# Kernel tuning notes

Hardware: AMD Instinct MI355X
Metric: run time of the kernel (lower is better)

Reference implementation:

```python
import jax, jax.numpy as jnp
import numpy as np

MAX_DISP = 4  # max_displacement
PAD = MAX_DISP
ODIM = 2 * MAX_DISP + 1  # 9 -> 81 cost-volume channels


def setup_inputs() -> dict:
    key = jax.random.key(0)
    k1, k2 = jax.random.split(key)
    B, C, H, W = 4, 256, 96, 192
    x1 = jax.random.normal(k1, (B, C, H, W), dtype=jnp.float32)
    x2 = jax.random.normal(k2, (B, C, H, W), dtype=jnp.float32)
    return {"x1": x1, "x2": x2}


def reference(x1, x2):
    B, C, H, W = x1.shape
    # zero-pad x2 spatially by PAD on each side (matches F.pad([pad]*4))
    x2p = jnp.pad(x2, ((0, 0), (0, 0), (PAD, PAD), (PAD, PAD)))
    cv = []
    for i in range(ODIM):          # fixed 9x9 displacement grid
        for j in range(ODIM):
            shifted = jax.lax.dynamic_slice(
                x2p, (0, 0, i, j), (B, C, H, W))
            # mean over channel dim -> [B, H, W]
            cv.append(jnp.mean(x1 * shifted, axis=1))
    return jnp.stack(cv, axis=1)  # [B, 81, H, W]
```

## Files before the change

### kernel.cpp

```cpp
#include <hip/hip_runtime.h>
#include <hip/hip_bf16.h>
#include <stddef.h>


#define NB 4
#define NC 256
#define HH 96
#define WW 192
#define CHW (HH * WW)
#define TW 16
#define TH 8
#define KC 32
#define NROWS 16
#define KS4 100
#define RS4 808
#define BUFSH (NROWS * RS4)

typedef __attribute__((ext_vector_type(8))) short bf16x8;
typedef __attribute__((ext_vector_type(4))) float f32x4;

union Frag { unsigned long long u[2]; unsigned int w[4]; bf16x8 v; };

__device__ __forceinline__ unsigned int pk2(float a, float b) {
    __hip_bfloat162 t = __float22bfloat162_rn(make_float2(a, b));
    union { __hip_bfloat162 h; unsigned int u; } c; c.h = t; return c.u;
}

__device__ __forceinline__ void lds_barrier() {
    __asm__ volatile("s_waitcnt lgkmcnt(0)\n\ts_barrier" ::: "memory");
}

__global__ __launch_bounds__(512, 4) void corr_mfma(
    const float* __restrict__ x1, const float* __restrict__ x2,
    float* __restrict__ out)
{
    __shared__ union {
        unsigned short xb[2][BUFSH];
        float band[TH][9][9][18];
    } lds;

    const int tid  = threadIdx.x;
    const int wv   = tid >> 6;
    const int lane = tid & 63;
    const int col  = lane & 15;
    const int q    = lane >> 4;

    const int nid = (blockIdx.x & 7) * 72 + (blockIdx.x >> 3);
    const int w0  = (nid % 12) * TW;
    const int h0  = ((nid / 12) % 12) * TH;
    const int b   = nid / 144;
    const int h   = h0 + wv;

    int  toff[3]; int tlds[3]; bool tok[3];
#pragma unroll
    for (int k = 0; k < 3; ++k) {
        int t   = tid + k * 512;
        int w2  = t % 12;
        int row = (t / 12) & 15;
        int cg  = t / 192;
        int gh  = h0 - 4 + row;
        int gw  = w0 - 4 + w2 * 2;
        tok[k]  = (gh >= 0) & (gh < HH) & (gw >= 0) & (gw < WW - 1);
        toff[k] = ((b * NC + cg * 4) * HH + gh) * WW + gw;
        tlds[k] = row * RS4 + cg * KS4 + w2 * 8;
    }
    const int x1off = ((b * NC + q * 8) * HH + h) * WW + w0 + col;

    f32x4 acc[9][2];
#pragma unroll
    for (int di = 0; di < 9; ++di) {
        acc[di][0] = (f32x4)0.0f;
        acc[di][1] = (f32x4)0.0f;
    }

    float pf[3][4][2];
    float pa[8];

#define STAGE_LOAD(KCV)                                                        \
    _Pragma("unroll")                                                          \
    for (int k = 0; k < 3; ++k) {                                              \
        int o = toff[k] + (KCV) * CHW;                                         \
        _Pragma("unroll")                                                      \
        for (int i = 0; i < 4; ++i) {                                          \
            float2 v = make_float2(0.f, 0.f);                                  \
            if (tok[k]) v = *(const float2*)&x2[o + i * CHW];                  \
            pf[k][i][0] = v.x; pf[k][i][1] = v.y;                              \
        }                                                                      \
    }

#define X1_LOAD(KCV)                                                           \
    _Pragma("unroll")                                                          \
    for (int j = 0; j < 8; ++j) pa[j] = x1[x1off + ((KCV) + j) * CHW];

    STAGE_LOAD(0)
    X1_LOAD(0)

    for (int ci = 0; ci < 8; ++ci) {
        unsigned short* xb = lds.xb[ci & 1];

#pragma unroll
        for (int k = 0; k < 3; ++k) {
#pragma unroll
            for (int p = 0; p < 2; ++p) {
                uint2 u = make_uint2(pk2(pf[k][0][p], pf[k][1][p]),
                                     pk2(pf[k][2][p], pf[k][3][p]));
                *(uint2*)&xb[tlds[k] + p * 4] = u;
            }
        }
        Frag fa;
#pragma unroll
        for (int jj = 0; jj < 4; ++jj) fa.w[jj] = pk2(pa[2 * jj], pa[2 * jj + 1]);

        if (ci < 7) { STAGE_LOAD((ci + 1) * KC) X1_LOAD((ci + 1) * KC) }

        lds_barrier();

#pragma unroll
        for (int di = 0; di < 9; ++di) {
            int rb = (wv + di) * RS4 + q * (2 * KS4) + col * 4;
            Frag b0, b1;
            b0.u[0] = *(const unsigned long long*)&xb[rb];
            b0.u[1] = *(const unsigned long long*)&xb[rb + KS4];
            b1.u[0] = *(const unsigned long long*)&xb[rb + 64];
            b1.u[1] = *(const unsigned long long*)&xb[rb + KS4 + 64];
            acc[di][0] = __builtin_amdgcn_mfma_f32_16x16x32_bf16(fa.v, b0.v, acc[di][0], 0, 0, 0);
            acc[di][1] = __builtin_amdgcn_mfma_f32_16x16x32_bf16(fa.v, b1.v, acc[di][1], 0, 0, 0);
        }
    }

    __syncthreads();

#pragma unroll
    for (int di = 0; di < 9; ++di)
#pragma unroll
        for (int half = 0; half < 2; ++half)
#pragma unroll
            for (int r = 0; r < 4; ++r) {
                int m  = q * 4 + r;
                int dj = half * 16 + col - m;
                if (dj >= 0 && dj < 9)
                    lds.band[wv][di][dj][m] = acc[di][half][r];
            }
    __syncthreads();

    const float scale = 1.0f / 256.0f;
#pragma unroll
    for (int it = 0; it < 21; ++it) {
        int combo = it * 4 + q;
        if (combo < 81) {
            float v = lds.band[wv][combo / 9][combo % 9][col];
            out[((size_t)((b * 81 + combo) * HH + h)) * WW + w0 + col] = v * scale;
        }
    }
}

extern "C" void kernel_launch(void* const* d_in, const int* in_sizes, int n_in,
                              void* d_out, int out_size, void* d_ws, size_t ws_size,
                              hipStream_t stream) {
    const float* x1 = (const float*)d_in[0];
    const float* x2 = (const float*)d_in[1];
    float* out = (float*)d_out;

    corr_mfma<<<dim3(576), dim3(512), 0, stream>>>(x1, x2, out);
}
```

Measured before the change: 261.9 us.

## Single-buffer LDS, float4 x2 loads, 3D grid, relaxed launch bounds

```diff
diff --git a/kernel.cpp b/kernel.cpp
--- a/kernel.cpp
+++ b/kernel.cpp
@@ -14,7 +14,7 @@
 #define NROWS 16
 #define KS4 100
 #define RS4 808
-#define BUFSH (NROWS * RS4)
+#define XBI4(row, kg, n) ((row) * RS4 + (kg) * KS4 + (n) * 4)
 
 typedef __attribute__((ext_vector_type(8))) short bf16x8;
 typedef __attribute__((ext_vector_type(4))) float f32x4;
@@ -30,12 +30,12 @@
     __asm__ volatile("s_waitcnt lgkmcnt(0)\n\ts_barrier" ::: "memory");
 }
 
-__global__ __launch_bounds__(512, 4) void corr_mfma(
+__global__ __launch_bounds__(512, 1) void corr_mfma(
     const float* __restrict__ x1, const float* __restrict__ x2,
     float* __restrict__ out)
 {
     __shared__ union {
-        unsigned short xb[2][BUFSH];
+        unsigned short xb[NROWS * RS4];
         float band[TH][9][9][18];
     } lds;
 
@@ -44,25 +44,24 @@
     const int lane = tid & 63;
     const int col  = lane & 15;
     const int q    = lane >> 4;
+    const int w0   = blockIdx.x * TW;
+    const int h0   = blockIdx.y * TH;
+    const int b    = blockIdx.z;
+    const int h    = h0 + wv;
 
-    const int nid = (blockIdx.x & 7) * 72 + (blockIdx.x >> 3);
-    const int w0  = (nid % 12) * TW;
-    const int h0  = ((nid / 12) % 12) * TH;
-    const int b   = nid / 144;
-    const int h   = h0 + wv;
-
-    int  toff[3]; int tlds[3]; bool tok[3];
+    const int ntask = (tid < 256) ? 2 : 1;
+    int toff[2]; int tlds[2]; bool tok[2];
 #pragma unroll
-    for (int k = 0; k < 3; ++k) {
-        int t   = tid + k * 512;
-        int w2  = t % 12;
-        int row = (t / 12) & 15;
-        int cg  = t / 192;
+    for (int k = 0; k < 2; ++k) {
+        int t   = (k == 0) ? tid : (tid + 512);
+        int seg = t % 6;
+        int row = (t / 6) & 15;
+        int cg  = t / 96;
         int gh  = h0 - 4 + row;
-        int gw  = w0 - 4 + w2 * 2;
-        tok[k]  = (gh >= 0) & (gh < HH) & (gw >= 0) & (gw < WW - 1);
+        int gw  = w0 - 4 + seg * 4;
+        tok[k]  = (gh >= 0) & (gh < HH) & (gw >= 0) & (gw + 3 < WW);
         toff[k] = ((b * NC + cg * 4) * HH + gh) * WW + gw;
-        tlds[k] = row * RS4 + cg * KS4 + w2 * 8;
+        tlds[k] = XBI4(row, cg, seg * 4);
     }
     const int x1off = ((b * NC + q * 8) * HH + h) * WW + w0 + col;
 
@@ -73,18 +72,21 @@
         acc[di][1] = (f32x4)0.0f;
     }
 
-    float pf[3][4][2];
+    float pf[2][4][4];
     float pa[8];
 
 #define STAGE_LOAD(KCV)                                                        \
     _Pragma("unroll")                                                          \
-    for (int k = 0; k < 3; ++k) {                                              \
-        int o = toff[k] + (KCV) * CHW;                                         \
-        _Pragma("unroll")                                                      \
-        for (int i = 0; i < 4; ++i) {                                          \
-            float2 v = make_float2(0.f, 0.f);                                  \
-            if (tok[k]) v = *(const float2*)&x2[o + i * CHW];                  \
-            pf[k][i][0] = v.x; pf[k][i][1] = v.y;                              \
+    for (int k = 0; k < 2; ++k) {                                              \
+        if (k < ntask) {                                                       \
+            int o = toff[k] + (KCV) * CHW;                                     \
+            _Pragma("unroll")                                                  \
+            for (int i = 0; i < 4; ++i) {                                      \
+                float4 v = make_float4(0.f, 0.f, 0.f, 0.f);                    \
+                if (tok[k]) v = *(const float4*)&x2[o + i * CHW];              \
+                pf[k][i][0] = v.x; pf[k][i][1] = v.y;                          \
+                pf[k][i][2] = v.z; pf[k][i][3] = v.w;                          \
+            }                                                                  \
         }                                                                      \
     }
 
@@ -96,39 +98,39 @@
     X1_LOAD(0)
 
     for (int ci = 0; ci < 8; ++ci) {
-        unsigned short* xb = lds.xb[ci & 1];
-
 #pragma unroll
-        for (int k = 0; k < 3; ++k) {
+        for (int k = 0; k < 2; ++k) {
+            if (k < ntask) {
 #pragma unroll
-            for (int p = 0; p < 2; ++p) {
-                uint2 u = make_uint2(pk2(pf[k][0][p], pf[k][1][p]),
-                                     pk2(pf[k][2][p], pf[k][3][p]));
-                *(uint2*)&xb[tlds[k] + p * 4] = u;
+                for (int p = 0; p < 4; ++p) {
+                    uint2 u = make_uint2(pk2(pf[k][0][p], pf[k][1][p]),
+                                         pk2(pf[k][2][p], pf[k][3][p]));
+                    *(uint2*)&lds.xb[tlds[k] + p * 4] = u;
+                }
             }
         }
         Frag fa;
 #pragma unroll
         for (int jj = 0; jj < 4; ++jj) fa.w[jj] = pk2(pa[2 * jj], pa[2 * jj + 1]);
 
+        lds_barrier();
+
         if (ci < 7) { STAGE_LOAD((ci + 1) * KC) X1_LOAD((ci + 1) * KC) }
-
-        lds_barrier();
 
 #pragma unroll
         for (int di = 0; di < 9; ++di) {
-            int rb = (wv + di) * RS4 + q * (2 * KS4) + col * 4;
+            int rb = XBI4(wv + di, 2 * q, col);
             Frag b0, b1;
-            b0.u[0] = *(const unsigned long long*)&xb[rb];
-            b0.u[1] = *(const unsigned long long*)&xb[rb + KS4];
-            b1.u[0] = *(const unsigned long long*)&xb[rb + 64];
-            b1.u[1] = *(const unsigned long long*)&xb[rb + KS4 + 64];
+            b0.u[0] = *(const unsigned long long*)&lds.xb[rb];
+            b0.u[1] = *(const unsigned long long*)&lds.xb[rb + KS4];
+            b1.u[0] = *(const unsigned long long*)&lds.xb[rb + 64];
+            b1.u[1] = *(const unsigned long long*)&lds.xb[rb + KS4 + 64];
             acc[di][0] = __builtin_amdgcn_mfma_f32_16x16x32_bf16(fa.v, b0.v, acc[di][0], 0, 0, 0);
             acc[di][1] = __builtin_amdgcn_mfma_f32_16x16x32_bf16(fa.v, b1.v, acc[di][1], 0, 0, 0);
         }
+
+        lds_barrier();
     }
-
-    __syncthreads();
 
 #pragma unroll
     for (int di = 0; di < 9; ++di)
@@ -141,7 +143,7 @@
                 if (dj >= 0 && dj < 9)
                     lds.band[wv][di][dj][m] = acc[di][half][r];
             }
-    __syncthreads();
+    lds_barrier();
 
     const float scale = 1.0f / 256.0f;
 #pragma unroll
@@ -161,5 +163,6 @@
     const float* x2 = (const float*)d_in[1];
     float* out = (float*)d_out;
 
-    corr_mfma<<<dim3(576), dim3(512), 0, stream>>>(x1, x2, out);
+    dim3 grid(WW / TW, HH / TH, NB);
+    corr_mfma<<<grid, 512, 0, stream>>>(x1, x2, out);
 }
```

After: 255.3 us. 2.5% less time.
